# Optimization experiments

Measured on AMD Instinct MI355X. Metric: run time of the kernel, lower is better.

The kernel has to match this reference:

```python
import jax, jax.numpy as jnp
import numpy as np

N_BOXES, N_VIEWS, C_FEAT, HF, WF = 256, 6, 256, 116, 200
IMG_H, IMG_W = 928, 1600
EPS = 1e-8


def setup_inputs() -> dict:
    key = jax.random.key(0)
    k1, k2, k3 = jax.random.split(key, 3)
    # Boxes: centers in front of the cameras so many (box, view) pairs are valid.
    xy = jax.random.uniform(k1, (N_BOXES, 2), minval=-8.0, maxval=8.0)
    z = jax.random.uniform(k2, (N_BOXES, 1), minval=1.0, maxval=40.0)
    rest = jax.random.normal(k3, (N_BOXES, 4)) * 0.5 + 2.0  # l, w, h, heading (unused by loss)
    pred_boxes_3d = jnp.concatenate([xy[:, :1], xy[:, 1:2], z, rest], axis=1).astype(jnp.float32)
    feats = jax.random.normal(jax.random.fold_in(key, 1), (N_VIEWS, C_FEAT, HF, WF), dtype=jnp.float32)
    # Intrinsics: fx=fy=1000, cx=800, cy=464; third row [0,0,1].
    K_one = jnp.array([[1000.0, 0.0, 800.0], [0.0, 1000.0, 464.0], [0.0, 0.0, 1.0]], dtype=jnp.float32)
    K = jnp.broadcast_to(K_one, (N_VIEWS, 3, 3))
    # Extrinsics: identity camera poses (camera at origin looking +z).
    T = jnp.broadcast_to(jnp.eye(4, dtype=jnp.float32), (N_VIEWS, 4, 4))
    img_sizes = jnp.broadcast_to(jnp.array([IMG_H, IMG_W], dtype=jnp.int32), (N_VIEWS, 2))
    return {"pred_boxes_3d": pred_boxes_3d, "feats": feats, "K": K, "T": T, "img_sizes": img_sizes}


def reference(pred_boxes_3d, feats, K, T, img_sizes):
    N = pred_boxes_3d.shape[0]
    V, C, Hf, Wf = feats.shape
    centers = pred_boxes_3d[:, :3]                                   # (N, 3)
    R, t = T[:, :3, :3], T[:, :3, 3]
    p_cam = jnp.einsum('vij,nj->nvi', R, centers) + t[None]          # (N, V, 3)
    p_2d = jnp.einsum('vij,nvj->nvi', K, p_cam)                      # (N, V, 3)
    z = p_cam[..., 2]
    u = p_2d[..., 0] / p_2d[..., 2]
    v = p_2d[..., 1] / z                                             # quirk: divides by point_cam z
    Wimg = img_sizes[:, 1].astype(jnp.float32)[None, :]              # (1, V)
    Himg = img_sizes[:, 0].astype(jnp.float32)[None, :]
    u_s = u * Wf / Wimg
    v_s = v * Hf / Himg
    u0 = jnp.floor(u_s).astype(jnp.int32)                            # u >= 0 on valid pairs -> floor == int()
    v0 = jnp.floor(v_s).astype(jnp.int32)
    valid = ((z > 0) & (u >= 0) & (u < Wimg) & (v >= 0) & (v < Himg)
             & (u0 < Wf - 1) & (v0 < Hf - 1))                        # (N, V)
    u0c = jnp.clip(u0, 0, Wf - 2)
    v0c = jnp.clip(v0, 0, Hf - 2)
    view = jnp.broadcast_to(jnp.arange(V)[None, :], (N, V))
    # mean of the 2x2 feature patch -> (N, V, C)
    fm = (feats[view, :, v0c, u0c] + feats[view, :, v0c, u0c + 1]
          + feats[view, :, v0c + 1, u0c] + feats[view, :, v0c + 1, u0c + 1]) * 0.25
    P = N * V
    fm_f = fm.reshape(P, C)
    valid_f = valid.reshape(P)
    # first valid pair in (box-major, view-minor) order is the stored anchor feature
    first = jnp.argmax(valid_f)
    stored = fm_f[first]                                             # (C,)
    cos = (fm_f @ stored) / (jnp.maximum(jnp.linalg.norm(fm_f, axis=1), EPS)
                             * jnp.maximum(jnp.linalg.norm(stored), EPS))
    loss_i = 1.0 - cos                                               # cosine_embedding_loss, target=1
    mask = valid_f & (jnp.arange(P) != first)                        # anchor pair itself contributes nothing
    n_pairs = jnp.sum(mask)
    total = jnp.sum(jnp.where(mask, loss_i, 0.0))
    return jnp.where(n_pairs > 0, total / jnp.maximum(n_pairs, 1).astype(total.dtype), jnp.zeros((), total.dtype))
```

## Files before the change

kernel.cpp:

```cpp
#include <hip/hip_runtime.h>
#include <math.h>

#define N_BOXES 256
#define N_VIEWS 6
#define C_FEAT 256
#define HF 116
#define WF 200
#define P_TOT (N_BOXES * N_VIEWS)
#define EPS_F 1e-8f

struct WsLayout {
    int   first;
    float norm_stored;
    int   count;
    int   pad;
    float stored[C_FEAT];
    int   packed[P_TOT];
    float loss[P_TOT];
};

__device__ __forceinline__ float wave_reduce_sum(float v) {
    #pragma unroll
    for (int off = 32; off > 0; off >>= 1)
        v += __shfl_down(v, off, 64);
    return v;
}

__global__ __launch_bounds__(256) void proj_kernel(
    const float* __restrict__ boxes,
    const float* __restrict__ feats,
    const float* __restrict__ Km,
    const float* __restrict__ Tm,
    const int*   __restrict__ img,
    WsLayout*    __restrict__ ws)
{
    __shared__ int   s_packed[P_TOT];
    __shared__ int   s_first;
    __shared__ int   s_cnt;
    __shared__ float s_red[4];
    const int tid = threadIdx.x;
    if (tid == 0) { s_first = 0x7fffffff; s_cnt = 0; }
    __syncthreads();

    int localmin = 0x7fffffff;
    int localcnt = 0;
    for (int p = tid; p < P_TOT; p += 256) {
        const int n = p / N_VIEWS, v = p % N_VIEWS;
        const float cx = boxes[n * 7 + 0];
        const float cy = boxes[n * 7 + 1];
        const float cz = boxes[n * 7 + 2];
        const float* Tv = Tm + v * 16;
        const float* Kv = Km + v * 9;
        float pc[3];
        #pragma unroll
        for (int i = 0; i < 3; ++i)
            pc[i] = Tv[i * 4 + 0] * cx + Tv[i * 4 + 1] * cy + Tv[i * 4 + 2] * cz + Tv[i * 4 + 3];
        float p2[3];
        #pragma unroll
        for (int i = 0; i < 3; ++i)
            p2[i] = Kv[i * 3 + 0] * pc[0] + Kv[i * 3 + 1] * pc[1] + Kv[i * 3 + 2] * pc[2];
        const float z  = pc[2];
        const float uu = p2[0] / p2[2];
        const float vv = p2[1] / z;
        const float Wimg = (float)img[v * 2 + 1];
        const float Himg = (float)img[v * 2 + 0];
        const float us = uu * (float)WF / Wimg;
        const float vs = vv * (float)HF / Himg;
        const int u0 = (int)floorf(us);
        const int v0 = (int)floorf(vs);
        const bool valid = (z > 0.f) && (uu >= 0.f) && (uu < Wimg) &&
                           (vv >= 0.f) && (vv < Himg) &&
                           (u0 < WF - 1) && (v0 < HF - 1);
        const int u0c = min(max(u0, 0), WF - 2);
        const int v0c = min(max(v0, 0), HF - 2);
        const int pk = u0c | (v0c << 9) | (valid ? (int)0x80000000 : 0);
        s_packed[p]   = pk;
        ws->packed[p] = pk;
        if (valid) {
            ++localcnt;
            if (p < localmin) localmin = p;
        }
    }
    if (localmin != 0x7fffffff) atomicMin(&s_first, localmin);
    if (localcnt) atomicAdd(&s_cnt, localcnt);
    __syncthreads();

    const bool any_valid = (s_first != 0x7fffffff);
    const int first = any_valid ? s_first : 0;
    if (tid == 0) {
        ws->first = first;
        ws->count = s_cnt - (any_valid ? 1 : 0);
    }

    const int pk = s_packed[first];
    const int x = pk & 0x1ff, y = (pk >> 9) & 0x7f;
    const int v = first % N_VIEWS;
    const float* base = feats + ((size_t)(v * C_FEAT + tid) * HF + y) * WF + x;
    const float fm = 0.25f * (base[0] + base[1] + base[WF] + base[WF + 1]);
    ws->stored[tid] = fm;

    float s = wave_reduce_sum(fm * fm);
    const int lane = tid & 63, wave = tid >> 6;
    if (lane == 0) s_red[wave] = s;
    __syncthreads();
    if (tid == 0) {
        const float nsq = s_red[0] + s_red[1] + s_red[2] + s_red[3];
        ws->norm_stored = fmaxf(sqrtf(nsq), EPS_F);
    }
}

__global__ __launch_bounds__(256) void gather_kernel(
    const float* __restrict__ feats,
    WsLayout*    __restrict__ ws)
{
    const int lane = threadIdx.x & 63;
    const int wave = threadIdx.x >> 6;
    const int p    = blockIdx.x * 4 + wave;

    const int first = ws->first;
    const int pk    = ws->packed[p];
    const bool active = (pk < 0) && (p != first);

    float dot = 0.f, nsq = 0.f;
    if (active) {
        const int x = pk & 0x1ff, y = (pk >> 9) & 0x7f;
        const int v = p % N_VIEWS;
        const float* base0 = feats + ((size_t)(v * C_FEAT) * HF + y) * WF + x;
        #pragma unroll
        for (int j = 0; j < 4; ++j) {
            const int c = lane + 64 * j;
            const float* b = base0 + (size_t)c * (HF * WF);
            const float fm = 0.25f * (b[0] + b[1] + b[WF] + b[WF + 1]);
            const float s  = ws->stored[c];
            dot += fm * s;
            nsq += fm * fm;
        }
    }
    dot = wave_reduce_sum(dot);
    nsq = wave_reduce_sum(nsq);

    if (lane == 0) {
        float l = 0.f;
        if (active)
            l = 1.0f - dot / (fmaxf(sqrtf(nsq), EPS_F) * ws->norm_stored);
        ws->loss[p] = l;
    }
}

__global__ __launch_bounds__(256) void finish_kernel(
    const WsLayout* __restrict__ ws,
    float*          __restrict__ out)
{
    __shared__ float s_red[4];
    const int tid = threadIdx.x;
    float s = 0.f;
    for (int p = tid; p < P_TOT; p += 256) s += ws->loss[p];
    s = wave_reduce_sum(s);
    const int lane = tid & 63, wave = tid >> 6;
    if (lane == 0) s_red[wave] = s;
    __syncthreads();
    if (tid == 0) {
        const float total = s_red[0] + s_red[1] + s_red[2] + s_red[3];
        const int   cnt   = ws->count;
        out[0] = (cnt > 0) ? total / (float)cnt : 0.0f;
    }
}

extern "C" void kernel_launch(void* const* d_in, const int* in_sizes, int n_in,
                              void* d_out, int out_size, void* d_ws, size_t ws_size,
                              hipStream_t stream) {
    const float* boxes = (const float*)d_in[0];
    const float* feats = (const float*)d_in[1];
    const float* Km    = (const float*)d_in[2];
    const float* Tm    = (const float*)d_in[3];
    const int*   img   = (const int*)d_in[4];
    float* out = (float*)d_out;
    WsLayout* ws = (WsLayout*)d_ws;

    hipLaunchKernelGGL(proj_kernel, dim3(1), dim3(256), 0, stream,
                       boxes, feats, Km, Tm, img, ws);
    hipLaunchKernelGGL(gather_kernel, dim3(P_TOT / 4), dim3(256), 0, stream,
                       feats, ws);
    hipLaunchKernelGGL(finish_kernel, dim3(1), dim3(256), 0, stream,
                       ws, out);
}
```

Measured before the change: 211.5 us.

## Fuse projection into gather kernel by recomputing projection per block

```diff
diff --git a/kernel.cpp b/kernel.cpp
--- a/kernel.cpp
+++ b/kernel.cpp
@@ -10,12 +10,8 @@
 #define EPS_F 1e-8f
 
 struct WsLayout {
-    int   first;
-    float norm_stored;
     int   count;
-    int   pad;
-    float stored[C_FEAT];
-    int   packed[P_TOT];
+    int   pad[15];
     float loss[P_TOT];
 };
 
@@ -26,7 +22,40 @@
     return v;
 }
 
-__global__ __launch_bounds__(256) void proj_kernel(
+__device__ __forceinline__ int project_pack(
+    const float* __restrict__ boxes, const float* __restrict__ Km,
+    const float* __restrict__ Tm, const int* __restrict__ img, int p)
+{
+    const int n = p / N_VIEWS, v = p - n * N_VIEWS;
+    const float cx = boxes[n * 7 + 0];
+    const float cy = boxes[n * 7 + 1];
+    const float cz = boxes[n * 7 + 2];
+    const float* Tv = Tm + v * 16;
+    const float* Kv = Km + v * 9;
+    float pc[3];
+    #pragma unroll
+    for (int i = 0; i < 3; ++i)
+        pc[i] = Tv[i * 4 + 0] * cx + Tv[i * 4 + 1] * cy + Tv[i * 4 + 2] * cz + Tv[i * 4 + 3];
+    float p2[3];
+    #pragma unroll
+    for (int i = 0; i < 3; ++i)
+        p2[i] = Kv[i * 3 + 0] * pc[0] + Kv[i * 3 + 1] * pc[1] + Kv[i * 3 + 2] * pc[2];
+    const float z  = pc[2];
+    const float uu = p2[0] / p2[2];
+    const float vv = p2[1] / z;
+    const float Wimg = (float)img[v * 2 + 1];
+    const float Himg = (float)img[v * 2 + 0];
+    const int u0 = (int)floorf(uu * (float)WF / Wimg);
+    const int v0 = (int)floorf(vv * (float)HF / Himg);
+    const bool valid = (z > 0.f) && (uu >= 0.f) && (uu < Wimg) &&
+                       (vv >= 0.f) && (vv < Himg) &&
+                       (u0 < WF - 1) && (v0 < HF - 1);
+    const int u0c = min(max(u0, 0), WF - 2);
+    const int v0c = min(max(v0, 0), HF - 2);
+    return u0c | (v0c << 9) | (valid ? (int)0x80000000 : 0);
+}
+
+__global__ __launch_bounds__(256) void fused_kernel(
     const float* __restrict__ boxes,
     const float* __restrict__ feats,
     const float* __restrict__ Km,
@@ -34,115 +63,67 @@
     const int*   __restrict__ img,
     WsLayout*    __restrict__ ws)
 {
-    __shared__ int   s_packed[P_TOT];
-    __shared__ int   s_first;
-    __shared__ int   s_cnt;
-    __shared__ float s_red[4];
-    const int tid = threadIdx.x;
-    if (tid == 0) { s_first = 0x7fffffff; s_cnt = 0; }
-    __syncthreads();
+    const int tid  = threadIdx.x;
+    const int lane = tid & 63;
+    const int wave = tid >> 6;
 
     int localmin = 0x7fffffff;
     int localcnt = 0;
-    for (int p = tid; p < P_TOT; p += 256) {
-        const int n = p / N_VIEWS, v = p % N_VIEWS;
-        const float cx = boxes[n * 7 + 0];
-        const float cy = boxes[n * 7 + 1];
-        const float cz = boxes[n * 7 + 2];
-        const float* Tv = Tm + v * 16;
-        const float* Kv = Km + v * 9;
-        float pc[3];
-        #pragma unroll
-        for (int i = 0; i < 3; ++i)
-            pc[i] = Tv[i * 4 + 0] * cx + Tv[i * 4 + 1] * cy + Tv[i * 4 + 2] * cz + Tv[i * 4 + 3];
-        float p2[3];
-        #pragma unroll
-        for (int i = 0; i < 3; ++i)
-            p2[i] = Kv[i * 3 + 0] * pc[0] + Kv[i * 3 + 1] * pc[1] + Kv[i * 3 + 2] * pc[2];
-        const float z  = pc[2];
-        const float uu = p2[0] / p2[2];
-        const float vv = p2[1] / z;
-        const float Wimg = (float)img[v * 2 + 1];
-        const float Himg = (float)img[v * 2 + 0];
-        const float us = uu * (float)WF / Wimg;
-        const float vs = vv * (float)HF / Himg;
-        const int u0 = (int)floorf(us);
-        const int v0 = (int)floorf(vs);
-        const bool valid = (z > 0.f) && (uu >= 0.f) && (uu < Wimg) &&
-                           (vv >= 0.f) && (vv < Himg) &&
-                           (u0 < WF - 1) && (v0 < HF - 1);
-        const int u0c = min(max(u0, 0), WF - 2);
-        const int v0c = min(max(v0, 0), HF - 2);
-        const int pk = u0c | (v0c << 9) | (valid ? (int)0x80000000 : 0);
-        s_packed[p]   = pk;
-        ws->packed[p] = pk;
-        if (valid) {
-            ++localcnt;
-            if (p < localmin) localmin = p;
-        }
+    #pragma unroll
+    for (int i = 0; i < P_TOT / 256; ++i) {
+        const int p  = tid + 256 * i;
+        const int pk = project_pack(boxes, Km, Tm, img, p);
+        if (pk < 0) { ++localcnt; if (p < localmin) localmin = p; }
     }
-    if (localmin != 0x7fffffff) atomicMin(&s_first, localmin);
-    if (localcnt) atomicAdd(&s_cnt, localcnt);
+    #pragma unroll
+    for (int off = 32; off > 0; off >>= 1) {
+        localmin = min(localmin, __shfl_down(localmin, off, 64));
+        localcnt += __shfl_down(localcnt, off, 64);
+    }
+    __shared__ int s_min[4], s_cnt[4];
+    if (lane == 0) { s_min[wave] = localmin; s_cnt[wave] = localcnt; }
     __syncthreads();
+    const int gmin = min(min(s_min[0], s_min[1]), min(s_min[2], s_min[3]));
+    const int gcnt = s_cnt[0] + s_cnt[1] + s_cnt[2] + s_cnt[3];
+    const bool any_valid = (gmin != 0x7fffffff);
+    const int first = any_valid ? gmin : 0;
 
-    const bool any_valid = (s_first != 0x7fffffff);
-    const int first = any_valid ? s_first : 0;
-    if (tid == 0) {
-        ws->first = first;
-        ws->count = s_cnt - (any_valid ? 1 : 0);
-    }
+    if (blockIdx.x == 0 && tid == 0)
+        ws->count = gcnt - (any_valid ? 1 : 0);
 
-    const int pk = s_packed[first];
-    const int x = pk & 0x1ff, y = (pk >> 9) & 0x7f;
-    const int v = first % N_VIEWS;
-    const float* base = feats + ((size_t)(v * C_FEAT + tid) * HF + y) * WF + x;
-    const float fm = 0.25f * (base[0] + base[1] + base[WF] + base[WF + 1]);
-    ws->stored[tid] = fm;
+    const int p = blockIdx.x * 4 + wave;
+    const int pk_p = project_pack(boxes, Km, Tm, img, p);
+    const int pk_f = project_pack(boxes, Km, Tm, img, first);
+    const bool active = (pk_p < 0) && (p != first);
 
-    float s = wave_reduce_sum(fm * fm);
-    const int lane = tid & 63, wave = tid >> 6;
-    if (lane == 0) s_red[wave] = s;
-    __syncthreads();
-    if (tid == 0) {
-        const float nsq = s_red[0] + s_red[1] + s_red[2] + s_red[3];
-        ws->norm_stored = fmaxf(sqrtf(nsq), EPS_F);
-    }
-}
-
-__global__ __launch_bounds__(256) void gather_kernel(
-    const float* __restrict__ feats,
-    WsLayout*    __restrict__ ws)
-{
-    const int lane = threadIdx.x & 63;
-    const int wave = threadIdx.x >> 6;
-    const int p    = blockIdx.x * 4 + wave;
-
-    const int first = ws->first;
-    const int pk    = ws->packed[p];
-    const bool active = (pk < 0) && (p != first);
-
-    float dot = 0.f, nsq = 0.f;
+    float dot = 0.f, nsq = 0.f, snsq = 0.f;
     if (active) {
-        const int x = pk & 0x1ff, y = (pk >> 9) & 0x7f;
-        const int v = p % N_VIEWS;
-        const float* base0 = feats + ((size_t)(v * C_FEAT) * HF + y) * WF + x;
+        const int xp = pk_p & 0x1ff, yp = (pk_p >> 9) & 0x7f;
+        const int xf = pk_f & 0x1ff, yf = (pk_f >> 9) & 0x7f;
+        const int vp = p % N_VIEWS;
+        const int vf = first % N_VIEWS;
+        const float* basep = feats + ((size_t)(vp * C_FEAT) * HF + yp) * WF + xp;
+        const float* basef = feats + ((size_t)(vf * C_FEAT) * HF + yf) * WF + xf;
         #pragma unroll
         for (int j = 0; j < 4; ++j) {
             const int c = lane + 64 * j;
-            const float* b = base0 + (size_t)c * (HF * WF);
-            const float fm = 0.25f * (b[0] + b[1] + b[WF] + b[WF + 1]);
-            const float s  = ws->stored[c];
-            dot += fm * s;
-            nsq += fm * fm;
+            const float* bp = basep + (size_t)c * (HF * WF);
+            const float* bf = basef + (size_t)c * (HF * WF);
+            const float fmp = 0.25f * (bp[0] + bp[1] + bp[WF] + bp[WF + 1]);
+            const float fmf = 0.25f * (bf[0] + bf[1] + bf[WF] + bf[WF + 1]);
+            dot  += fmp * fmf;
+            nsq  += fmp * fmp;
+            snsq += fmf * fmf;
         }
     }
-    dot = wave_reduce_sum(dot);
-    nsq = wave_reduce_sum(nsq);
+    dot  = wave_reduce_sum(dot);
+    nsq  = wave_reduce_sum(nsq);
+    snsq = wave_reduce_sum(snsq);
 
     if (lane == 0) {
         float l = 0.f;
         if (active)
-            l = 1.0f - dot / (fmaxf(sqrtf(nsq), EPS_F) * ws->norm_stored);
+            l = 1.0f - dot / (fmaxf(sqrtf(nsq), EPS_F) * fmaxf(sqrtf(snsq), EPS_F));
         ws->loss[p] = l;
     }
 }
@@ -154,7 +135,8 @@
     __shared__ float s_red[4];
     const int tid = threadIdx.x;
     float s = 0.f;
-    for (int p = tid; p < P_TOT; p += 256) s += ws->loss[p];
+    #pragma unroll
+    for (int i = 0; i < P_TOT / 256; ++i) s += ws->loss[tid + 256 * i];
     s = wave_reduce_sum(s);
     const int lane = tid & 63, wave = tid >> 6;
     if (lane == 0) s_red[wave] = s;
@@ -177,10 +159,8 @@
     float* out = (float*)d_out;
     WsLayout* ws = (WsLayout*)d_ws;
 
-    hipLaunchKernelGGL(proj_kernel, dim3(1), dim3(256), 0, stream,
+    hipLaunchKernelGGL(fused_kernel, dim3(P_TOT / 4), dim3(256), 0, stream,
                        boxes, feats, Km, Tm, img, ws);
-    hipLaunchKernelGGL(gather_kernel, dim3(P_TOT / 4), dim3(256), 0, stream,
-                       feats, ws);
     hipLaunchKernelGGL(finish_kernel, dim3(1), dim3(256), 0, stream,
                        ws, out);
 }
```

Result: faster. 205.8 us (-2.7%).
